# Kernel tuning notes

Measured on AMD Instinct MI355X. Metric: run time of the kernel, lower is better.

Reference implementation:

```python
import jax, jax.numpy as jnp
import numpy as np

D_MODEL = 256
NUM_HEADS = 8
HEAD_DIM = D_MODEL // NUM_HEADS
SCALE = HEAD_DIM ** -0.5
LN_EPS = 1e-5


def setup_inputs() -> dict:
    key = jax.random.key(0)
    ks = jax.random.split(key, 16)
    B, N, H, W = 1, 8, 16, 16
    s = 1.0 / np.sqrt(D_MODEL)
    inp = {
        'features': jax.random.normal(ks[0], (B, N, H, W, D_MODEL), jnp.float32),
        'pointmaps': jax.random.normal(ks[1], (B, N, H, W, 3), jnp.float32),
        'Wq': jax.random.normal(ks[2], (D_MODEL, D_MODEL), jnp.float32) * s,
        'bq': jnp.zeros((D_MODEL,), jnp.float32),
        'Wk': jax.random.normal(ks[3], (D_MODEL, D_MODEL), jnp.float32) * s,
        'bk': jnp.zeros((D_MODEL,), jnp.float32),
        'Wv': jax.random.normal(ks[4], (D_MODEL, D_MODEL), jnp.float32) * s,
        'bv': jnp.zeros((D_MODEL,), jnp.float32),
        'Wo': jax.random.normal(ks[5], (D_MODEL, D_MODEL), jnp.float32) * s,
        'bo': jnp.zeros((D_MODEL,), jnp.float32),
        'beta': jnp.asarray(1.0, jnp.float32),
        'k_w1': jax.random.normal(ks[6], (32, 1), jnp.float32) * 0.1,
        'k_b1': jnp.zeros((32,), jnp.float32),
        'k_w2': jax.random.normal(ks[7], (1, 32), jnp.float32) * 0.1,
        'k_b2': jnp.full((1,), -1.0, jnp.float32),
        'ln_g': jnp.ones((D_MODEL,), jnp.float32),
        'ln_b': jnp.zeros((D_MODEL,), jnp.float32),
    }
    return inp


def _gasa_forward(features, pointmaps, Wq, bq, Wk, bk, Wv, bv, Wo, bo,
                  beta, k_w1, k_b1, k_w2, k_b2, ln_g, ln_b):
    B, N, H, W, D = features.shape
    L = N * H * W
    x = features.reshape(B, L, D)

    # QKV projections (torch Linear: x @ W.T + b)
    Q = (x @ Wq.T + bq).reshape(B, L, NUM_HEADS, HEAD_DIM).transpose(0, 2, 1, 3)
    K = (x @ Wk.T + bk).reshape(B, L, NUM_HEADS, HEAD_DIM).transpose(0, 2, 1, 3)
    V = (x @ Wv.T + bv).reshape(B, L, NUM_HEADS, HEAD_DIM).transpose(0, 2, 1, 3)

    # semantic scores [B, h, L, L]
    scores = jnp.einsum('bhqd,bhkd->bhqk', Q, K) * SCALE

    # geometric bias: pairwise 3D distances + tiny MLP kernel, clamp to [-10, 0]
    pts = pointmaps.reshape(B, L, 3)
    diff = pts[:, :, None, :] - pts[:, None, :, :]           # [B, L, L, 3]
    sq = jnp.sum(diff * diff, axis=-1)                        # [B, L, L]
    dist = jnp.where(sq > 0, jnp.sqrt(jnp.where(sq > 0, sq, 1.0)), 0.0)
    h = jax.nn.relu(dist[..., None] * k_w1[:, 0] + k_b1)      # [B, L, L, 32]
    bias = h @ k_w2[0] + k_b2[0]                              # [B, L, L]
    bias = jnp.clip(bias, -10.0, 0.0)

    scores = scores + beta * bias[:, None, :, :]
    probs = jax.nn.softmax(scores, axis=-1)
    out = jnp.einsum('bhqk,bhkd->bhqd', probs, V)
    out = out.transpose(0, 2, 1, 3).reshape(B, L, D)
    out = out @ Wo.T + bo

    # residual + LayerNorm
    y = x + out
    mu = jnp.mean(y, axis=-1, keepdims=True)
    var = jnp.mean(jnp.square(y - mu), axis=-1, keepdims=True)
    y = (y - mu) * jax.lax.rsqrt(var + LN_EPS) * ln_g + ln_b
    return y.reshape(B, N, H, W, D)


def reference(features, pointmaps, Wq, bq, Wk, bk, Wv, bv, Wo, bo,
              beta, k_w1, k_b1, k_w2, k_b2, ln_g, ln_b):
    return _gasa_forward(features, pointmaps, Wq, bq, Wk, bk, Wv, bv, Wo, bo,
                         beta, k_w1, k_b1, k_w2, k_b2, ln_g, ln_b)
```

## Files before the change

### kernel.cpp

```cpp
#include <hip/hip_runtime.h>
#include <math.h>

#define L_SEQ 2048
#define DM    256
#define NH    8
#define HD    32

typedef __attribute__((ext_vector_type(8))) short bf16x8;
typedef __attribute__((ext_vector_type(4))) float f32x4;

__device__ __forceinline__ unsigned short f2bf(float f) {
    unsigned int u = __builtin_bit_cast(unsigned int, f);
    u += 0x7fff + ((u >> 16) & 1);
    return (unsigned short)(u >> 16);
}

__device__ __forceinline__ bf16x8 ld8_cvt(const float* __restrict__ p) {
    float4 u = *(const float4*)p;
    float4 v = *(const float4*)(p + 4);
    union { unsigned int i[4]; bf16x8 h; } r;
    r.i[0] = __builtin_amdgcn_perm(__builtin_bit_cast(unsigned int, u.y),
                                   __builtin_bit_cast(unsigned int, u.x), 0x07060302);
    r.i[1] = __builtin_amdgcn_perm(__builtin_bit_cast(unsigned int, u.w),
                                   __builtin_bit_cast(unsigned int, u.z), 0x07060302);
    r.i[2] = __builtin_amdgcn_perm(__builtin_bit_cast(unsigned int, v.y),
                                   __builtin_bit_cast(unsigned int, v.x), 0x07060302);
    r.i[3] = __builtin_amdgcn_perm(__builtin_bit_cast(unsigned int, v.w),
                                   __builtin_bit_cast(unsigned int, v.z), 0x07060302);
    return r.h;
}

__global__ __launch_bounds__(256) void fused_front(
    const float* __restrict__ x, const float* __restrict__ pts,
    const float* __restrict__ Wq, const float* __restrict__ bq,
    const float* __restrict__ Wk, const float* __restrict__ bk,
    const float* __restrict__ Wv, const float* __restrict__ bv,
    const float* __restrict__ k_w1, const float* __restrict__ k_b1,
    const float* __restrict__ k_w2, const float* __restrict__ k_b2,
    const float* __restrict__ beta_p,
    unsigned short* __restrict__ Qb, unsigned short* __restrict__ Kb,
    unsigned short* __restrict__ Vt, unsigned short* __restrict__ biasP)
{
    const int bx = blockIdx.x;
    const int t = threadIdx.x;

    if (bx < 384) {
        const int z  = bx >> 7;
        const int r0 = (bx & 127) << 4;
        const int w = t >> 6, lane = t & 63, quad = lane >> 4, c = lane & 15;
        const int c0 = w * 64;
        const float* Wm  = (z == 0) ? Wq : (z == 1) ? Wk : Wv;
        const float* bia = (z == 0) ? bq : (z == 1) ? bk : bv;

        f32x4 acc[4] = {};
        for (int kt = 0; kt < 8; ++kt) {
            bf16x8 a = ld8_cvt(x + (size_t)(r0 + c) * DM + kt * 32 + quad * 8);
#pragma unroll
            for (int ct = 0; ct < 4; ++ct) {
                bf16x8 b = ld8_cvt(Wm + (size_t)(c0 + ct * 16 + c) * DM + kt * 32 + quad * 8);
                acc[ct] = __builtin_amdgcn_mfma_f32_16x16x32_bf16(a, b, acc[ct], 0, 0, 0);
            }
        }
        if (z < 2) {
            unsigned short* out = (z == 0) ? Qb : Kb;
#pragma unroll
            for (int ct = 0; ct < 4; ++ct) {
                float bc = bia[c0 + ct * 16 + c];
#pragma unroll
                for (int reg = 0; reg < 4; ++reg) {
                    int r = r0 + quad * 4 + reg;
                    out[(size_t)r * DM + c0 + ct * 16 + c] = f2bf(acc[ct][reg] + bc);
                }
            }
        } else {
#pragma unroll
            for (int ct = 0; ct < 4; ++ct) {
                int col = c0 + ct * 16 + c;
                float bc = bia[col];
#pragma unroll
                for (int reg = 0; reg < 4; ++reg) {
                    int key = r0 + quad * 4 + reg;
                    int loc = key & 31;
                    int pos = (key & ~31) + 2 * (loc & 15) + (loc >> 4);
                    Vt[(size_t)col * L_SEQ + pos] = f2bf(acc[ct][reg] + bc);
                }
            }
        }
    } else {
        const int b = bx - 384;
        const int i = b >> 1;
        const int p0 = ((b & 1) * 256 + t) * 4;
        const float xi = pts[i * 3], yi = pts[i * 3 + 1], zi = pts[i * 3 + 2];
        const float beta = beta_p[0], b2 = k_b2[0];

        float dist[4];
#pragma unroll
        for (int v = 0; v < 4; ++v) {
            int p = p0 + v, loc = p & 31, base = p & ~31;
            int k = base + (loc >> 1) + 16 * (loc & 1);
            float dx = xi - pts[k * 3], dy = yi - pts[k * 3 + 1], dz = zi - pts[k * 3 + 2];
            dist[v] = sqrtf(dx * dx + dy * dy + dz * dz);
        }
        float s[4] = {0.f, 0.f, 0.f, 0.f};
#pragma unroll
        for (int n = 0; n < 32; ++n) {
            float w1 = k_w1[n], b1 = k_b1[n], w2 = k_w2[n];
#pragma unroll
            for (int v = 0; v < 4; ++v) s[v] += fmaxf(fmaf(dist[v], w1, b1), 0.f) * w2;
        }
        ushort4 o; unsigned short* po = (unsigned short*)&o;
#pragma unroll
        for (int v = 0; v < 4; ++v)
            po[v] = f2bf(fminf(fmaxf(s[v] + b2, -10.f), 0.f) * beta);
        *(ushort4*)(biasP + (size_t)i * L_SEQ + p0) = o;
    }
}

__global__ __launch_bounds__(256) void attn_mfma(
    const unsigned short* __restrict__ Qb, const unsigned short* __restrict__ Kb,
    const unsigned short* __restrict__ Vt, const unsigned short* __restrict__ biasP,
    unsigned short* __restrict__ Ab)
{
    __shared__ unsigned short Plds[4][32][40];
    __shared__ float Ol[4][32][36];
    __shared__ float Ll[4][32];
    const int t = threadIdx.x, w = t >> 6, lane = t & 63, quad = lane >> 4, c = lane & 15;
    const int h = blockIdx.y, r0 = blockIdx.x * 32;
    const int kbase = w * 512;
    const f32x4 Z = {};

    bf16x8 qf0 = *(const bf16x8*)(Qb + (size_t)(r0 + c) * DM + h * HD + quad * 8);
    bf16x8 qf1 = *(const bf16x8*)(Qb + (size_t)(r0 + 16 + c) * DM + h * HD + quad * 8);

    f32x4 O00 = {}, O01 = {}, O10 = {}, O11 = {};
    float l0[4] = {0.f,0.f,0.f,0.f}, l1[4] = {0.f,0.f,0.f,0.f};

    const float LOG2E = 1.4426950408889634f;
    const float C1 = 0.17677669529663687f * LOG2E;
    const float MC = -10.0f * LOG2E;

    const unsigned short* Kp  = Kb + (size_t)h * HD + quad * 8;
    const unsigned short* Vp0 = Vt + (size_t)(h * HD + c) * L_SEQ + quad * 8;
    const unsigned short* Vp1 = Vt + (size_t)(h * HD + 16 + c) * L_SEQ + quad * 8;
    const int br0 = r0 + quad * 4;

    bf16x8 kf0 = *(const bf16x8*)(Kp + (size_t)(kbase + c) * DM);
    bf16x8 kf1 = *(const bf16x8*)(Kp + (size_t)(kbase + 16 + c) * DM);
    bf16x8 vf0 = *(const bf16x8*)(Vp0 + kbase);
    bf16x8 vf1 = *(const bf16x8*)(Vp1 + kbase);
    unsigned int bu0[4], bu1[4];
#pragma unroll
    for (int reg = 0; reg < 4; ++reg) {
        bu0[reg] = *(const unsigned int*)(biasP + (size_t)(br0 + reg) * L_SEQ + kbase + c * 2);
        bu1[reg] = *(const unsigned int*)(biasP + (size_t)(br0 + 16 + reg) * L_SEQ + kbase + c * 2);
    }

    for (int kt = 0; kt < 16; ++kt) {
        const int kn = kbase + (kt + 1) * 32;
        bf16x8 nk0 = kf0, nk1 = kf1, nv0 = vf0, nv1 = vf1;
        unsigned int nbu0[4], nbu1[4];
#pragma unroll
        for (int reg = 0; reg < 4; ++reg) { nbu0[reg] = bu0[reg]; nbu1[reg] = bu1[reg]; }
        if (kt < 15) {
            nk0 = *(const bf16x8*)(Kp + (size_t)(kn + c) * DM);
            nk1 = *(const bf16x8*)(Kp + (size_t)(kn + 16 + c) * DM);
            nv0 = *(const bf16x8*)(Vp0 + kn);
            nv1 = *(const bf16x8*)(Vp1 + kn);
#pragma unroll
            for (int reg = 0; reg < 4; ++reg) {
                nbu0[reg] = *(const unsigned int*)(biasP + (size_t)(br0 + reg) * L_SEQ + kn + c * 2);
                nbu1[reg] = *(const unsigned int*)(biasP + (size_t)(br0 + 16 + reg) * L_SEQ + kn + c * 2);
            }
        }

        f32x4 S00 = __builtin_amdgcn_mfma_f32_16x16x32_bf16(qf0, kf0, Z, 0, 0, 0);
        f32x4 S01 = __builtin_amdgcn_mfma_f32_16x16x32_bf16(qf0, kf1, Z, 0, 0, 0);
        f32x4 S10 = __builtin_amdgcn_mfma_f32_16x16x32_bf16(qf1, kf0, Z, 0, 0, 0);
        f32x4 S11 = __builtin_amdgcn_mfma_f32_16x16x32_bf16(qf1, kf1, Z, 0, 0, 0);

#pragma unroll
        for (int reg = 0; reg < 4; ++reg) {
            unsigned int u = bu0[reg];
            float blo = __builtin_bit_cast(float, u << 16);
            float bhi = __builtin_bit_cast(float, u & 0xffff0000u);
            float p0 = __builtin_exp2f(fmaf(S00[reg], C1, fmaf(blo, LOG2E, MC)));
            float p1 = __builtin_exp2f(fmaf(S01[reg], C1, fmaf(bhi, LOG2E, MC)));
            l0[reg] += p0 + p1;
            unsigned int pb = __builtin_amdgcn_perm(
                __builtin_bit_cast(unsigned int, p1),
                __builtin_bit_cast(unsigned int, p0), 0x07060302);
            *(unsigned int*)&Plds[w][quad * 4 + reg][c * 2] = pb;

            u = bu1[reg];
            blo = __builtin_bit_cast(float, u << 16);
            bhi = __builtin_bit_cast(float, u & 0xffff0000u);
            p0 = __builtin_exp2f(fmaf(S10[reg], C1, fmaf(blo, LOG2E, MC)));
            p1 = __builtin_exp2f(fmaf(S11[reg], C1, fmaf(bhi, LOG2E, MC)));
            l1[reg] += p0 + p1;
            pb = __builtin_amdgcn_perm(
                __builtin_bit_cast(unsigned int, p1),
                __builtin_bit_cast(unsigned int, p0), 0x07060302);
            *(unsigned int*)&Plds[w][16 + quad * 4 + reg][c * 2] = pb;
        }

        bf16x8 pa0 = *(const bf16x8*)&Plds[w][c][quad * 8];
        bf16x8 pa1 = *(const bf16x8*)&Plds[w][16 + c][quad * 8];
        O00 = __builtin_amdgcn_mfma_f32_16x16x32_bf16(pa0, vf0, O00, 0, 0, 0);
        O01 = __builtin_amdgcn_mfma_f32_16x16x32_bf16(pa0, vf1, O01, 0, 0, 0);
        O10 = __builtin_amdgcn_mfma_f32_16x16x32_bf16(pa1, vf0, O10, 0, 0, 0);
        O11 = __builtin_amdgcn_mfma_f32_16x16x32_bf16(pa1, vf1, O11, 0, 0, 0);

        kf0 = nk0; kf1 = nk1; vf0 = nv0; vf1 = nv1;
#pragma unroll
        for (int reg = 0; reg < 4; ++reg) { bu0[reg] = nbu0[reg]; bu1[reg] = nbu1[reg]; }
    }

#pragma unroll
    for (int off = 1; off < 16; off <<= 1) {
#pragma unroll
        for (int reg = 0; reg < 4; ++reg) {
            l0[reg] += __shfl_xor(l0[reg], off, 16);
            l1[reg] += __shfl_xor(l1[reg], off, 16);
        }
    }
#pragma unroll
    for (int reg = 0; reg < 4; ++reg) {
        int row = quad * 4 + reg;
        Ol[w][row][c]           = O00[reg];
        Ol[w][row][16 + c]      = O01[reg];
        Ol[w][row + 16][c]      = O10[reg];
        Ol[w][row + 16][16 + c] = O11[reg];
    }
    if (c == 0) {
#pragma unroll
        for (int reg = 0; reg < 4; ++reg) {
            Ll[w][quad * 4 + reg]      = l0[reg];
            Ll[w][quad * 4 + reg + 16] = l1[reg];
        }
    }
    __syncthreads();
    {
        int row = t >> 3, c4 = (t & 7) * 4;
        float4 a = *(const float4*)&Ol[0][row][c4];
        float4 b = *(const float4*)&Ol[1][row][c4];
        float4 d = *(const float4*)&Ol[2][row][c4];
        float4 e = *(const float4*)&Ol[3][row][c4];
        float inv = 1.0f / (Ll[0][row] + Ll[1][row] + Ll[2][row] + Ll[3][row]);
        ushort4 ob;
        ob.x = f2bf((a.x + b.x + d.x + e.x) * inv);
        ob.y = f2bf((a.y + b.y + d.y + e.y) * inv);
        ob.z = f2bf((a.z + b.z + d.z + e.z) * inv);
        ob.w = f2bf((a.w + b.w + d.w + e.w) * inv);
        *(ushort4*)(Ab + (size_t)(r0 + row) * DM + h * HD + c4) = ob;
    }
}

__global__ __launch_bounds__(256) void proj_ln(
    const unsigned short* __restrict__ Ab, const float* __restrict__ Wo,
    const float* __restrict__ bo, const float* __restrict__ feat,
    const float* __restrict__ ln_g, const float* __restrict__ ln_b,
    float* __restrict__ out)
{
    __shared__ float red1[4][16], red2[4][16];
    const int t = threadIdx.x, w = t >> 6, lane = t & 63, quad = lane >> 4, c = lane & 15;
    const int r0 = blockIdx.x * 16, c0 = w * 64;

    f32x4 acc[4] = {};
    for (int kt = 0; kt < 8; ++kt) {
        bf16x8 a = *(const bf16x8*)(Ab + (size_t)(r0 + c) * DM + kt * 32 + quad * 8);
#pragma unroll
        for (int ct = 0; ct < 4; ++ct) {
            bf16x8 b = ld8_cvt(Wo + (size_t)(c0 + ct * 16 + c) * DM + kt * 32 + quad * 8);
            acc[ct] = __builtin_amdgcn_mfma_f32_16x16x32_bf16(a, b, acc[ct], 0, 0, 0);
        }
    }
    float y[4][4];
    float s1[4] = {0.f,0.f,0.f,0.f}, s2[4] = {0.f,0.f,0.f,0.f};
#pragma unroll
    for (int ct = 0; ct < 4; ++ct) {
        int col = c0 + ct * 16 + c;
        float bc = bo[col];
#pragma unroll
        for (int reg = 0; reg < 4; ++reg) {
            int r = r0 + quad * 4 + reg;
            float v = acc[ct][reg] + bc + feat[(size_t)r * DM + col];
            y[ct][reg] = v;
            s1[reg] += v; s2[reg] += v * v;
        }
    }
#pragma unroll
    for (int off = 1; off < 16; off <<= 1)
#pragma unroll
        for (int reg = 0; reg < 4; ++reg) {
            s1[reg] += __shfl_xor(s1[reg], off, 16);
            s2[reg] += __shfl_xor(s2[reg], off, 16);
        }
    if (c == 0)
#pragma unroll
        for (int reg = 0; reg < 4; ++reg) {
            red1[w][quad * 4 + reg] = s1[reg];
            red2[w][quad * 4 + reg] = s2[reg];
        }
    __syncthreads();
    float mu[4], rs[4];
#pragma unroll
    for (int reg = 0; reg < 4; ++reg) {
        int row = quad * 4 + reg;
        float a1 = red1[0][row] + red1[1][row] + red1[2][row] + red1[3][row];
        float a2 = red2[0][row] + red2[1][row] + red2[2][row] + red2[3][row];
        float m = a1 * (1.0f / 256.0f);
        mu[reg] = m;
        rs[reg] = rsqrtf(a2 * (1.0f / 256.0f) - m * m + 1e-5f);
    }
#pragma unroll
    for (int ct = 0; ct < 4; ++ct) {
        int col = c0 + ct * 16 + c;
        float g = ln_g[col], bb = ln_b[col];
#pragma unroll
        for (int reg = 0; reg < 4; ++reg) {
            int r = r0 + quad * 4 + reg;
            out[(size_t)r * DM + col] = (y[ct][reg] - mu[reg]) * rs[reg] * g + bb;
        }
    }
}

extern "C" void kernel_launch(void* const* d_in, const int* in_sizes, int n_in,
                              void* d_out, int out_size, void* d_ws, size_t ws_size,
                              hipStream_t stream) {
    (void)in_sizes; (void)n_in; (void)out_size; (void)ws_size;
    const float* features  = (const float*)d_in[0];
    const float* pointmaps = (const float*)d_in[1];
    const float* Wq = (const float*)d_in[2];  const float* bq = (const float*)d_in[3];
    const float* Wk = (const float*)d_in[4];  const float* bk = (const float*)d_in[5];
    const float* Wv = (const float*)d_in[6];  const float* bv = (const float*)d_in[7];
    const float* Wo = (const float*)d_in[8];  const float* bo = (const float*)d_in[9];
    const float* beta = (const float*)d_in[10];
    const float* k_w1 = (const float*)d_in[11]; const float* k_b1 = (const float*)d_in[12];
    const float* k_w2 = (const float*)d_in[13]; const float* k_b2 = (const float*)d_in[14];
    const float* ln_g = (const float*)d_in[15]; const float* ln_b = (const float*)d_in[16];
    float* out = (float*)d_out;

    char* W = (char*)d_ws;
    unsigned short* Qb    = (unsigned short*)(W);
    unsigned short* Kb    = (unsigned short*)(W + 1048576);
    unsigned short* Vt    = (unsigned short*)(W + 2097152);
    unsigned short* Ab    = (unsigned short*)(W + 3145728);
    unsigned short* biasP = (unsigned short*)(W + 4194304);

    fused_front<<<4480, 256, 0, stream>>>(features, pointmaps,
                                          Wq, bq, Wk, bk, Wv, bv,
                                          k_w1, k_b1, k_w2, k_b2, beta,
                                          Qb, Kb, Vt, biasP);
    attn_mfma <<<dim3(64, 8), 256, 0, stream>>>(Qb, Kb, Vt, biasP, Ab);
    proj_ln   <<<128,         256, 0, stream>>>(Ab, Wo, bo, features, ln_g, ln_b, out);
}
```

Measured before the change: 151.0 us.

## Pre-convert inputs to bf16 and replace distance MLP with interpolated lookup table

Adds a prep kernel that converts features and the four weight matrices to bf16 once, so the projection GEMMs load bf16 directly instead of converting fp32 on every tile load. The same kernel tabulates the 32-unit distance MLP bias (clamped, scaled by beta) over distances 0 to 16 at 1/256 steps. The bias blocks then read this table with linear interpolation instead of evaluating 32 neurons per pair. This adds one launch and extra workspace traffic. The table approximates the ReLU MLP, clamping distances above 16 and misplacing kinks between grid points, so accuracy depends on the input distance range.

```diff
diff --git a/kernel.cpp b/kernel.cpp
--- a/kernel.cpp
+++ b/kernel.cpp
@@ -15,29 +15,51 @@
     return (unsigned short)(u >> 16);
 }
 
-__device__ __forceinline__ bf16x8 ld8_cvt(const float* __restrict__ p) {
-    float4 u = *(const float4*)p;
-    float4 v = *(const float4*)(p + 4);
-    union { unsigned int i[4]; bf16x8 h; } r;
-    r.i[0] = __builtin_amdgcn_perm(__builtin_bit_cast(unsigned int, u.y),
-                                   __builtin_bit_cast(unsigned int, u.x), 0x07060302);
-    r.i[1] = __builtin_amdgcn_perm(__builtin_bit_cast(unsigned int, u.w),
-                                   __builtin_bit_cast(unsigned int, u.z), 0x07060302);
-    r.i[2] = __builtin_amdgcn_perm(__builtin_bit_cast(unsigned int, v.y),
-                                   __builtin_bit_cast(unsigned int, v.x), 0x07060302);
-    r.i[3] = __builtin_amdgcn_perm(__builtin_bit_cast(unsigned int, v.w),
-                                   __builtin_bit_cast(unsigned int, v.z), 0x07060302);
-    return r.h;
-}
-
-__global__ __launch_bounds__(256) void fused_front(
-    const float* __restrict__ x, const float* __restrict__ pts,
-    const float* __restrict__ Wq, const float* __restrict__ bq,
-    const float* __restrict__ Wk, const float* __restrict__ bk,
-    const float* __restrict__ Wv, const float* __restrict__ bv,
+__global__ __launch_bounds__(256) void prep(
+    const float* __restrict__ x,  const float* __restrict__ wq,
+    const float* __restrict__ wk, const float* __restrict__ wv,
+    const float* __restrict__ wo,
     const float* __restrict__ k_w1, const float* __restrict__ k_b1,
     const float* __restrict__ k_w2, const float* __restrict__ k_b2,
     const float* __restrict__ beta_p,
+    unsigned short* __restrict__ xb,  unsigned short* __restrict__ wqb,
+    unsigned short* __restrict__ wkb, unsigned short* __restrict__ wvb,
+    unsigned short* __restrict__ wob, float* __restrict__ T)
+{
+    const int bx = blockIdx.x, t = threadIdx.x;
+    if (bx < 384) {
+        int e = (bx * 256 + t) * 8;
+        const float* src; unsigned short* dst; int off;
+        if      (e < 524288) { src = x;  dst = xb;  off = e; }
+        else if (e < 589824) { src = wq; dst = wqb; off = e - 524288; }
+        else if (e < 655360) { src = wk; dst = wkb; off = e - 589824; }
+        else if (e < 720896) { src = wv; dst = wvb; off = e - 655360; }
+        else                 { src = wo; dst = wob; off = e - 720896; }
+        float4 u = *(const float4*)(src + off);
+        float4 v = *(const float4*)(src + off + 4);
+        ushort4 a, b;
+        a.x = f2bf(u.x); a.y = f2bf(u.y); a.z = f2bf(u.z); a.w = f2bf(u.w);
+        b.x = f2bf(v.x); b.y = f2bf(v.y); b.z = f2bf(v.z); b.w = f2bf(v.w);
+        *(ushort4*)(dst + off)     = a;
+        *(ushort4*)(dst + off + 4) = b;
+    } else {
+        int n = (bx - 384) * 256 + t;
+        float d = (float)n * (1.0f / 256.0f);
+        float s = 0.f;
+#pragma unroll
+        for (int k = 0; k < 32; ++k)
+            s += fmaxf(fmaf(d, k_w1[k], k_b1[k]), 0.f) * k_w2[k];
+        s = fminf(fmaxf(s + k_b2[0], -10.f), 0.f);
+        T[n] = beta_p[0] * s;
+    }
+}
+
+__global__ __launch_bounds__(256) void fused_front(
+    const unsigned short* __restrict__ xb, const float* __restrict__ pts,
+    const unsigned short* __restrict__ wqb, const float* __restrict__ bq,
+    const unsigned short* __restrict__ wkb, const float* __restrict__ bk,
+    const unsigned short* __restrict__ wvb, const float* __restrict__ bv,
+    const float* __restrict__ T,
     unsigned short* __restrict__ Qb, unsigned short* __restrict__ Kb,
     unsigned short* __restrict__ Vt, unsigned short* __restrict__ biasP)
 {
@@ -49,15 +71,15 @@
         const int r0 = (bx & 127) << 4;
         const int w = t >> 6, lane = t & 63, quad = lane >> 4, c = lane & 15;
         const int c0 = w * 64;
-        const float* Wm  = (z == 0) ? Wq : (z == 1) ? Wk : Wv;
-        const float* bia = (z == 0) ? bq : (z == 1) ? bk : bv;
+        const unsigned short* Wm = (z == 0) ? wqb : (z == 1) ? wkb : wvb;
+        const float* bia         = (z == 0) ? bq  : (z == 1) ? bk  : bv;
 
         f32x4 acc[4] = {};
         for (int kt = 0; kt < 8; ++kt) {
-            bf16x8 a = ld8_cvt(x + (size_t)(r0 + c) * DM + kt * 32 + quad * 8);
+            bf16x8 a = *(const bf16x8*)(xb + (size_t)(r0 + c) * DM + kt * 32 + quad * 8);
 #pragma unroll
             for (int ct = 0; ct < 4; ++ct) {
-                bf16x8 b = ld8_cvt(Wm + (size_t)(c0 + ct * 16 + c) * DM + kt * 32 + quad * 8);
+                bf16x8 b = *(const bf16x8*)(Wm + (size_t)(c0 + ct * 16 + c) * DM + kt * 32 + quad * 8);
                 acc[ct] = __builtin_amdgcn_mfma_f32_16x16x32_bf16(a, b, acc[ct], 0, 0, 0);
             }
         }
@@ -91,27 +113,20 @@
         const int i = b >> 1;
         const int p0 = ((b & 1) * 256 + t) * 4;
         const float xi = pts[i * 3], yi = pts[i * 3 + 1], zi = pts[i * 3 + 2];
-        const float beta = beta_p[0], b2 = k_b2[0];
-
-        float dist[4];
+
+        ushort4 o; unsigned short* po = (unsigned short*)&o;
 #pragma unroll
         for (int v = 0; v < 4; ++v) {
             int p = p0 + v, loc = p & 31, base = p & ~31;
             int k = base + (loc >> 1) + 16 * (loc & 1);
             float dx = xi - pts[k * 3], dy = yi - pts[k * 3 + 1], dz = zi - pts[k * 3 + 2];
-            dist[v] = sqrtf(dx * dx + dy * dy + dz * dz);
-        }
-        float s[4] = {0.f, 0.f, 0.f, 0.f};
-#pragma unroll
-        for (int n = 0; n < 32; ++n) {
-            float w1 = k_w1[n], b1 = k_b1[n], w2 = k_w2[n];
-#pragma unroll
-            for (int v = 0; v < 4; ++v) s[v] += fmaxf(fmaf(dist[v], w1, b1), 0.f) * w2;
-        }
-        ushort4 o; unsigned short* po = (unsigned short*)&o;
-#pragma unroll
-        for (int v = 0; v < 4; ++v)
-            po[v] = f2bf(fminf(fmaxf(s[v] + b2, -10.f), 0.f) * beta);
+            float dist = sqrtf(dx * dx + dy * dy + dz * dz);
+            float fn = dist * 256.0f;
+            int n = (int)fn; n = (n > 4094) ? 4094 : n;
+            float fr = fn - (float)n;
+            float t0 = T[n], t1 = T[n + 1];
+            po[v] = f2bf(fmaf(fr, t1 - t0, t0));
+        }
         *(ushort4*)(biasP + (size_t)i * L_SEQ + p0) = o;
     }
 }
@@ -256,7 +271,7 @@
 }
 
 __global__ __launch_bounds__(256) void proj_ln(
-    const unsigned short* __restrict__ Ab, const float* __restrict__ Wo,
+    const unsigned short* __restrict__ Ab, const unsigned short* __restrict__ Wob,
     const float* __restrict__ bo, const float* __restrict__ feat,
     const float* __restrict__ ln_g, const float* __restrict__ ln_b,
     float* __restrict__ out)
@@ -270,7 +285,7 @@
         bf16x8 a = *(const bf16x8*)(Ab + (size_t)(r0 + c) * DM + kt * 32 + quad * 8);
 #pragma unroll
         for (int ct = 0; ct < 4; ++ct) {
-            bf16x8 b = ld8_cvt(Wo + (size_t)(c0 + ct * 16 + c) * DM + kt * 32 + quad * 8);
+            bf16x8 b = *(const bf16x8*)(Wob + (size_t)(c0 + ct * 16 + c) * DM + kt * 32 + quad * 8);
             acc[ct] = __builtin_amdgcn_mfma_f32_16x16x32_bf16(a, b, acc[ct], 0, 0, 0);
         }
     }
@@ -341,16 +356,24 @@
     float* out = (float*)d_out;
 
     char* W = (char*)d_ws;
-    unsigned short* Qb    = (unsigned short*)(W);
-    unsigned short* Kb    = (unsigned short*)(W + 1048576);
-    unsigned short* Vt    = (unsigned short*)(W + 2097152);
-    unsigned short* Ab    = (unsigned short*)(W + 3145728);
-    unsigned short* biasP = (unsigned short*)(W + 4194304);
-
-    fused_front<<<4480, 256, 0, stream>>>(features, pointmaps,
-                                          Wq, bq, Wk, bk, Wv, bv,
-                                          k_w1, k_b1, k_w2, k_b2, beta,
+    unsigned short* xb    = (unsigned short*)(W);
+    unsigned short* Wqb   = (unsigned short*)(W + 1048576);
+    unsigned short* Wkb   = (unsigned short*)(W + 1179648);
+    unsigned short* Wvb   = (unsigned short*)(W + 1310720);
+    unsigned short* Wob   = (unsigned short*)(W + 1441792);
+    float*          T     = (float*)        (W + 1572864);
+    unsigned short* Qb    = (unsigned short*)(W + 1589248);
+    unsigned short* Kb    = (unsigned short*)(W + 2637824);
+    unsigned short* Vt    = (unsigned short*)(W + 3686400);
+    unsigned short* Ab    = (unsigned short*)(W + 4734976);
+    unsigned short* biasP = (unsigned short*)(W + 5783552);
+
+    prep       <<<400, 256, 0, stream>>>(features, Wq, Wk, Wv, Wo,
+                                         k_w1, k_b1, k_w2, k_b2, beta,
+                                         xb, Wqb, Wkb, Wvb, Wob, T);
+    fused_front<<<4480, 256, 0, stream>>>(xb, pointmaps,
+                                          Wqb, bq, Wkb, bk, Wvb, bv, T,
                                           Qb, Kb, Vt, biasP);
-    attn_mfma <<<dim3(64, 8), 256, 0, stream>>>(Qb, Kb, Vt, biasP, Ab);
-    proj_ln   <<<128,         256, 0, stream>>>(Ab, Wo, bo, features, ln_g, ln_b, out);
-}
+    attn_mfma  <<<dim3(64, 8), 256, 0, stream>>>(Qb, Kb, Vt, biasP, Ab);
+    proj_ln    <<<128,         256, 0, stream>>>(Ab, Wob, bo, features, ln_g, ln_b, out);
+}
```

Result: faster. 139.2 us (-7.8%).
